# Kernel tuning notes

Hardware: AMD Instinct MI355X
Metric: run time of the kernel (lower is better)

Reference implementation:

```python
import jax, jax.numpy as jnp
import numpy as np

D = 2048          # input_dim == dec_hidden_size
S = 16384         # src_time_steps
H = 250           # projection hidden (hard-coded in module)


def setup_inputs() -> dict:
    key = jax.random.key(0)
    ks = jax.random.split(key, 12)
    sc_d = 1.0 / np.sqrt(D)
    sc_3d = 1.0 / np.sqrt(3 * D)
    sc_h = 1.0 / np.sqrt(H)
    return {
        "s_prev": jax.random.normal(ks[0], (1, 1, D), jnp.float32),
        "enc_hs": jax.random.normal(ks[1], (1, S, D), jnp.float32),
        "cur_men_rep": jax.random.normal(ks[2], (1, 1, D), jnp.float32),
        "src_mask": jax.random.randint(ks[3], (1, S), 0, 2, jnp.int32),
        "W_info": jax.random.normal(ks[4], (D, D), jnp.float32) * sc_d,
        "W_ctx": jax.random.normal(ks[5], (D, D), jnp.float32) * sc_d,
        "W_q": jax.random.normal(ks[6], (D, D), jnp.float32) * sc_d,
        "b_q": jnp.zeros((D,), jnp.float32),
        "W_p1": jax.random.normal(ks[7], (H, 3 * D), jnp.float32) * sc_3d,
        "b_p1": jnp.zeros((H,), jnp.float32),
        "W_p2": jax.random.normal(ks[8], (1, H), jnp.float32) * sc_h,
        "b_p2": jnp.zeros((1,), jnp.float32),
    }


def reference(s_prev, enc_hs, cur_men_rep, src_mask,
              W_info, W_ctx, W_q, b_q, W_p1, b_p1, W_p2, b_p2):
    # dh = linear_info(cur_men_rep): [1,1,D]; uh = linear_ctx(enc_hs): [1,S,D]
    dh = jnp.einsum('bqe,de->bqd', cur_men_rep, W_info)
    uh = jnp.einsum('bse,de->bsd', enc_hs, W_ctx)
    wq = jnp.einsum('bqe,de->bqd', s_prev, W_q) + b_q
    # cat(uh, wq.repeat, dh.repeat) -> tanh : [1,S,3D]
    wquh = jnp.tanh(jnp.concatenate(
        [uh, jnp.broadcast_to(wq, uh.shape), jnp.broadcast_to(dh, uh.shape)],
        axis=2))
    # projection: Linear(3D,250) -> Dropout(eval: identity) -> ReLU -> Linear(250,1)
    h = jax.nn.relu(jnp.einsum('bsk,hk->bsh', wquh, W_p1) + b_p1)
    scores = (jnp.einsum('bsh,oh->bso', h, W_p2) + b_p2).squeeze()   # [S] (B=1)
    scores = jnp.where(src_mask.squeeze().astype(bool), -jnp.inf, scores)
    attn = jax.nn.softmax(scores, axis=-1)                            # [S]
    ctx = jnp.sum(enc_hs * attn[None, :, None], axis=1)               # [1,D]
    return attn, ctx
```

## Files before the change

kernel.cpp:

```cpp
#include <hip/hip_runtime.h>
#include <hip/hip_bf16.h>
#include <stdint.h>

#define DD 2048
#define SS 16384
#define HH 250
#define GEMMB_GRID 264

typedef __attribute__((ext_vector_type(8))) short bf16x8;
typedef __attribute__((ext_vector_type(4))) short bf16x4;
typedef __attribute__((ext_vector_type(4))) float f32x4;

__device__ __forceinline__ unsigned short f2bf(float f){
  union { float f; uint32_t u; } v; v.f = f;
  uint32_t u = v.u;
  return (unsigned short)((u + 0x7fffu + ((u >> 16) & 1u)) >> 16);
}
__device__ __forceinline__ float bf2f(unsigned short h){
  union { uint32_t u; float f; } v; v.u = ((uint32_t)h) << 16; return v.f;
}
__device__ __forceinline__ bf16x4 pk4(float4 a){
  bf16x4 v;
  v[0]=(short)f2bf(a.x); v[1]=(short)f2bf(a.y); v[2]=(short)f2bf(a.z); v[3]=(short)f2bf(a.w);
  return v;
}
__device__ __forceinline__ float fast_tanh(float x){
  return 1.0f - 2.0f / (1.0f + __expf(2.0f * x));
}
__device__ __forceinline__ void gl_lds16(const void* g, void* l){
  __builtin_amdgcn_global_load_lds((const __attribute__((address_space(1))) void*)g,
                                   (__attribute__((address_space(3))) void*)l, 16, 0, 0);
}

__global__ __launch_bounds__(1024) void scan_kernel(const int* __restrict__ mask,
                                                    int* __restrict__ idx,
                                                    int* __restrict__ cpos,
                                                    int* __restrict__ mcount)
{
  __shared__ int wsum[16];
  const int t = threadIdx.x, lane = t & 63, w = t >> 6;
  int running = 0;
  for(int k = 0; k < 16; k++){
    const int e = k * 1024 + t;
    const int m = (mask[e] == 0);
    unsigned long long bal = __ballot(m);
    if(lane == 0) wsum[w] = __popcll(bal);
    __syncthreads();
    int wpre = 0;
    for(int i = 0; i < w; i++) wpre += wsum[i];
    int tot = wpre;
    for(int i = w; i < 16; i++) tot += wsum[i];
    const int lpre = __popcll(bal & ((1ull << lane) - 1ull));
    const int pos = running + wpre + lpre;
    if(m){ idx[pos] = e; cpos[e] = pos; } else cpos[e] = -1;
    running += tot;
    __syncthreads();
  }
  if(t == 0){
    mcount[0] = running;
    mcount[1] = (running + 255) & ~255;
    mcount[2] = (running + 63) & ~63;
  }
}

__global__ __launch_bounds__(256) void mega_kernel(
    const float* __restrict__ enc, unsigned short* __restrict__ encb,
    const float* __restrict__ W_ctx, unsigned short* __restrict__ wctxb,
    const float* __restrict__ W_p1, unsigned short* __restrict__ wp1ab,
    const float* __restrict__ s_prev, const float* __restrict__ cmr,
    const float* __restrict__ Wq, const float* __restrict__ bq,
    const float* __restrict__ Winfo,
    float* __restrict__ twq, float* __restrict__ tdh)
{
  const int b = blockIdx.x, t = threadIdx.x;
  if(b < 2048){
    const float4* in4 = (const float4*)enc;
    bf16x4* out4 = (bf16x4*)encb;
    const int gt = b * 256 + t;
    const int S = 524288;
    #pragma unroll
    for(int k = 0; k < 4; k++){
      int i0 = gt + (4 * k + 0) * S, i1 = gt + (4 * k + 1) * S;
      int i2 = gt + (4 * k + 2) * S, i3 = gt + (4 * k + 3) * S;
      float4 a = in4[i0], c = in4[i1], d = in4[i2], e = in4[i3];
      out4[i0] = pk4(a); out4[i1] = pk4(c); out4[i2] = pk4(d); out4[i3] = pk4(e);
    }
  } else if(b < 2304){
    const float4* in4 = (const float4*)W_ctx;
    bf16x4* out4 = (bf16x4*)wctxb;
    const int gt = (b - 2048) * 256 + t;
    const int S = 65536;
    #pragma unroll
    for(int k = 0; k < 4; k++){
      int i0 = gt + (4 * k + 0) * S, i1 = gt + (4 * k + 1) * S;
      int i2 = gt + (4 * k + 2) * S, i3 = gt + (4 * k + 3) * S;
      float4 a = in4[i0], c = in4[i1], d = in4[i2], e = in4[i3];
      out4[i0] = pk4(a); out4[i1] = pk4(c); out4[i2] = pk4(d); out4[i3] = pk4(e);
    }
  } else if(b < 2336){
    bf16x4* out4 = (bf16x4*)wp1ab;
    const int gt = (b - 2304) * 256 + t;
    const int S = 8192;
    #pragma unroll
    for(int k = 0; k < 16; k++){
      int i = gt + k * S;
      int row = i >> 9, col = i & 511;
      bf16x4 v;
      if(row < HH){
        float4 a = *(const float4*)(W_p1 + (size_t)row * (3 * DD) + (col << 2));
        v = pk4(a);
      } else {
        v[0] = 0; v[1] = 0; v[2] = 0; v[3] = 0;
      }
      out4[i] = v;
    }
  } else {
    int vb = b - 2336;
    int wid = t >> 6, lane = t & 63;
    bool isq = vb < 512;
    int r = (isq ? vb : vb - 512) * 4 + wid;
    const float* M = (isq ? Wq : Winfo) + (size_t)r * DD;
    const float* x = isq ? s_prev : cmr;
    float s = 0.f;
    for(int i = lane; i < DD; i += 64) s += M[i] * x[i];
    #pragma unroll
    for(int o = 32; o; o >>= 1) s += __shfl_xor(s, o);
    if(lane == 0){
      if(isq) twq[r] = fast_tanh(s + bq[r]);
      else    tdh[r] = fast_tanh(s);
    }
  }
}

__device__ __forceinline__ void stageA_idx(const unsigned short* __restrict__ g,
                                           const int* r2, int kt, char* ldsbase,
                                           int wid, int lane)
{
  const int srow = lane >> 3;
  const int c = (lane & 7) ^ srow;
  #pragma unroll
  for(int i = 0; i < 2; i++){
    int r8 = (wid * 2 + i) * 8;
    gl_lds16(g + (size_t)r2[i] * DD + kt + c * 8, ldsbase + r8 * 128);
  }
}
__device__ __forceinline__ void stage_half(const unsigned short* __restrict__ g,
                                           int grow0, int kt, char* ldsbase,
                                           int wid, int lane)
{
  const int srow = lane >> 3;
  const int c = (lane & 7) ^ srow;
  #pragma unroll
  for(int i = 0; i < 2; i++){
    int r8 = (wid * 2 + i) * 8;
    gl_lds16(g + (size_t)(grow0 + r8 + srow) * DD + kt + c * 8,
             ldsbase + r8 * 128);
  }
}
#define RDF(base, lr, kc) (*(const bf16x8*)((base) + (lr) * 128 + (((kc) * 16) ^ (((lr) & 7) << 4))))

__global__ __launch_bounds__(512, 2) void gemmA_kernel(
    const unsigned short* __restrict__ A, const int* __restrict__ idx,
    const unsigned short* __restrict__ B, const int* __restrict__ mcount,
    unsigned short* __restrict__ Ct,
    const float* __restrict__ wp1, const float* __restrict__ bp1,
    const float* __restrict__ twq, const float* __restrict__ tdh,
    float* __restrict__ bias2)
{
  const int tid = threadIdx.x, lane = tid & 63, wid = tid >> 6;
  if(blockIdx.x >= 512){
    int h = (blockIdx.x - 512) * 8 + wid;
    if(h >= HH){ if(lane == 0 && h < 256) bias2[h] = 0.f; return; }
    const float* r1 = wp1 + (size_t)h * (3 * DD) + DD;
    const float* r2 = wp1 + (size_t)h * (3 * DD) + 2 * DD;
    float s = 0.f;
    for(int i = lane; i < DD; i += 64) s += r1[i] * twq[i] + r2[i] * tdh[i];
    #pragma unroll
    for(int o = 32; o; o >>= 1) s += __shfl_xor(s, o);
    if(lane == 0) bias2[h] = s + bp1[h];
    return;
  }
  __shared__ alignas(128) char lds[131072];
  const int wm = wid >> 2, wn = wid & 3;
  const int slot = blockIdx.x >> 3;
  const int mt = (blockIdx.x & 7) + ((slot >> 3) << 3);
  const int n0 = (slot & 7) * 256;
  const int MT = mcount[1] >> 8;
  if(mt >= MT) return;
  const int m0 = mt * 256;
  const int frow = lane & 15, kch = lane >> 4;

  int ra0[2], ra1[2];
  {
    const int tot = mcount[0];
    const int srow = lane >> 3;
    #pragma unroll
    for(int i = 0; i < 2; i++){
      int r0 = m0 + (wid * 2 + i) * 8 + srow;
      int r1 = r0 + 128;
      ra0[i] = idx[r0 < tot ? r0 : tot - 1];
      ra1[i] = idx[r1 < tot ? r1 : tot - 1];
    }
  }

  f32x4 acc[8][4] = {};

  stageA_idx(A, ra0, 0, lds,         wid, lane);
  stageA_idx(A, ra1, 0, lds + 16384, wid, lane);
  stage_half(B, n0,        0, lds + 32768,         wid, lane);
  stage_half(B, n0 + 128,  0, lds + 49152,         wid, lane);
  stage_half(B, n0,       64, lds + 65536 + 32768, wid, lane);
  stage_half(B, n0 + 128, 64, lds + 65536 + 49152, wid, lane);
  asm volatile("s_waitcnt vmcnt(4)" ::: "memory");
  __builtin_amdgcn_s_barrier();

  #pragma unroll 2
  for(int t = 0; t < 32; t++){
    const int d = t & 1;
    char* Ab = lds + d * 65536;
    char* Bb = Ab + 32768;
    char* An = lds + (d ^ 1) * 65536;
    bf16x8 bfr[4][2];
    #pragma unroll
    for(int q = 0; q < 4; q++){
      if(q == 0){
        #pragma unroll
        for(int nr = 0; nr < 4; nr++){
          int row = wn * 64 + nr * 16 + frow;
          #pragma unroll
          for(int ks = 0; ks < 2; ks++) bfr[nr][ks] = RDF(Bb, row, ks * 4 + kch);
        }
      }
      bf16x8 afr[2][2];
      #pragma unroll
      for(int mi = 0; mi < 2; mi++){
        int row = wm * 128 + (q * 2 + mi) * 16 + frow;
        #pragma unroll
        for(int ks = 0; ks < 2; ks++) afr[mi][ks] = RDF(Ab, row, ks * 4 + kch);
      }
      if(q == 0){
        if(t + 1 < 32){
          stageA_idx(A, ra0, (t + 1) * 64, An,         wid, lane);
          stageA_idx(A, ra1, (t + 1) * 64, An + 16384, wid, lane);
        }
      } else if(q == 1){
        if(t + 2 < 32) stage_half(B, n0,       (t + 2) * 64, Bb,         wid, lane);
      } else if(q == 2){
        if(t + 2 < 32) stage_half(B, n0 + 128, (t + 2) * 64, Bb + 16384, wid, lane);
      }
      __builtin_amdgcn_s_barrier();
      __builtin_amdgcn_sched_barrier(0);
      __builtin_amdgcn_s_setprio(1);
      #pragma unroll
      for(int mi = 0; mi < 2; mi++)
        #pragma unroll
        for(int nr = 0; nr < 4; nr++)
          #pragma unroll
          for(int ks = 0; ks < 2; ks++)
            acc[q * 2 + mi][nr] = __builtin_amdgcn_mfma_f32_16x16x32_bf16(
                afr[mi][ks], bfr[nr][ks], acc[q * 2 + mi][nr], 0, 0, 0);
      __builtin_amdgcn_s_setprio(0);
      __builtin_amdgcn_sched_barrier(0);
      if(q == 3){
        if(t < 30)       asm volatile("s_waitcnt vmcnt(4)" ::: "memory");
        else if(t == 30) asm volatile("s_waitcnt vmcnt(0)" ::: "memory");
      }
      __builtin_amdgcn_s_barrier();
    }
  }

  const int r0 = m0 + wm * 128 + (lane >> 4) * 4;
  const int c0 = n0 + wn * 64 + frow;
  #pragma unroll
  for(int mr = 0; mr < 8; mr++)
    #pragma unroll
    for(int nr = 0; nr < 4; nr++)
      #pragma unroll
      for(int r = 0; r < 4; r++)
        Ct[(size_t)(r0 + mr * 16 + r) * DD + c0 + nr * 16] = f2bf(fast_tanh(acc[mr][nr][r]));
}

__global__ __launch_bounds__(512, 4) void gemmB_kernel(
    const unsigned short* __restrict__ A, const unsigned short* __restrict__ B,
    const int* __restrict__ mcount, const float* __restrict__ bias2,
    const float* __restrict__ w2, const float* __restrict__ bp2,
    float* __restrict__ attnc, float* __restrict__ Tpart)
{
  __shared__ alignas(128) char lds[81920];
  __shared__ float sred[8][32];
  const int tid = threadIdx.x, lane = tid & 63, wid = tid >> 6;
  const int wm = wid >> 2, wn = wid & 3;
  const int m0 = blockIdx.x * 64;
  const int mc0 = mcount[0], mc2 = mcount[2];
  if(m0 >= mc2){ if(tid == 0) Tpart[blockIdx.x] = 0.f; return; }
  const int frow = lane & 15, kch = lane >> 4;
  const int srow = lane >> 3, sc = ((lane & 7) ^ srow) * 8;

  f32x4 acc[2][4] = {};

  gl_lds16(A + (size_t)(m0 + wid * 8 + srow) * DD + sc, lds + wid * 1024);
  #pragma unroll
  for(int i = 0; i < 4; i++){
    int l = wid + 8 * i;
    gl_lds16(B + (size_t)(l * 8 + srow) * DD + sc,      lds + 16384 + l * 1024);
    gl_lds16(B + (size_t)(l * 8 + srow) * DD + 64 + sc, lds + 49152 + l * 1024);
  }
  asm volatile("s_waitcnt vmcnt(4)" ::: "memory");
  __builtin_amdgcn_s_barrier();

  #pragma unroll 2
  for(int t = 0; t < 32; t++){
    const int d = t & 1;
    char* Ab = lds + d * 8192;
    char* An = lds + (d ^ 1) * 8192;
    char* Bb = lds + 16384 + d * 32768;
    bf16x8 bfr[4][2], afr[2];
    #pragma unroll
    for(int q = 0; q < 2; q++){
      if(q == 0){
        #pragma unroll
        for(int nr = 0; nr < 4; nr++){
          int row = wn * 64 + nr * 16 + frow;
          #pragma unroll
          for(int ks = 0; ks < 2; ks++) bfr[nr][ks] = RDF(Bb, row, ks * 4 + kch);
        }
      }
      {
        int row = wm * 32 + q * 16 + frow;
        #pragma unroll
        for(int ks = 0; ks < 2; ks++) afr[ks] = RDF(Ab, row, ks * 4 + kch);
      }
      if(q == 0){
        if(t + 1 < 32)
          gl_lds16(A + (size_t)(m0 + wid * 8 + srow) * DD + (t + 1) * 64 + sc, An + wid * 1024);
      } else {
        if(t + 2 < 32){
          #pragma unroll
          for(int i = 0; i < 4; i++){
            int l = wid + 8 * i;
            gl_lds16(B + (size_t)(l * 8 + srow) * DD + (t + 2) * 64 + sc, Bb + l * 1024);
          }
        }
      }
      __builtin_amdgcn_s_barrier();
      __builtin_amdgcn_sched_barrier(0);
      __builtin_amdgcn_s_setprio(1);
      #pragma unroll
      for(int nr = 0; nr < 4; nr++)
        #pragma unroll
        for(int ks = 0; ks < 2; ks++)
          acc[q][nr] = __builtin_amdgcn_mfma_f32_16x16x32_bf16(afr[ks], bfr[nr][ks], acc[q][nr], 0, 0, 0);
      __builtin_amdgcn_s_setprio(0);
      __builtin_amdgcn_sched_barrier(0);
      if(q == 1){
        if(t < 30)       asm volatile("s_waitcnt vmcnt(4)" ::: "memory");
        else if(t == 30) asm volatile("s_waitcnt vmcnt(0)" ::: "memory");
      }
      __builtin_amdgcn_s_barrier();
    }
  }

  float w2v[4], b2v[4];
  #pragma unroll
  for(int in = 0; in < 4; in++){
    int n = wn * 64 + in * 16 + frow;
    w2v[in] = (n < HH) ? w2[n] : 0.f;
    b2v[in] = bias2[n];
  }
  #pragma unroll
  for(int mi = 0; mi < 2; mi++){
    #pragma unroll
    for(int r = 0; r < 4; r++){
      float s = 0.f;
      #pragma unroll
      for(int in = 0; in < 4; in++){
        float h = acc[mi][in][r] + b2v[in];
        s += (h > 0.f ? h : 0.f) * w2v[in];
      }
      s += __shfl_xor(s, 1); s += __shfl_xor(s, 2);
      s += __shfl_xor(s, 4); s += __shfl_xor(s, 8);
      if(frow == 0) sred[wid][mi * 16 + (lane >> 4) * 4 + r] = s;
    }
  }
  __syncthreads();
  if(tid < 64){
    int wmr = tid >> 5, rr = tid & 31;
    float s = sred[wmr * 4][rr] + sred[wmr * 4 + 1][rr] + sred[wmr * 4 + 2][rr]
            + sred[wmr * 4 + 3][rr] + bp2[0];
    int j = m0 + tid;
    float e = (j < mc0) ? __expf(s) : 0.f;
    if(j < mc0) attnc[j] = e;
    #pragma unroll
    for(int o = 32; o; o >>= 1) e += __shfl_xor(e, o);
    if(tid == 0) Tpart[blockIdx.x] = e;
  }
}

__global__ __launch_bounds__(256) void normctx_kernel(
    const float* __restrict__ attnc, const int* __restrict__ cpos,
    const int* __restrict__ idx, const int* __restrict__ mcount,
    const float* __restrict__ Tpart, const unsigned short* __restrict__ encb,
    float* __restrict__ out, float* __restrict__ part)
{
  const int b = blockIdx.x, t = threadIdx.x;
  if(b < 64){
    __shared__ float sT;
    if(t == 0){
      float s = 0.f;
      for(int i = 0; i < GEMMB_GRID; i++) s += Tpart[i];
      sT = 1.0f / s;
    }
    __syncthreads();
    int i = b * 256 + t;
    int cp = cpos[i];
    out[i] = (cp >= 0) ? attnc[cp] * sT : 0.f;
  } else {
    const int bb = b - 64;
    const int mc0 = mcount[0];
    const int chunk = (mc0 + 255) >> 8;
    const int j0 = bb * chunk;
    const int j1 = min(j0 + chunk, mc0);
    float a[8] = {};
    for(int j = j0; j < j1; j++){
      float e = attnc[j];
      bf16x8 v = *(const bf16x8*)(encb + (size_t)idx[j] * DD + t * 8);
      #pragma unroll
      for(int k = 0; k < 8; k++) a[k] += e * bf2f((unsigned short)v[k]);
    }
    float* o = part + (size_t)bb * DD + t * 8;
    #pragma unroll
    for(int k = 0; k < 8; k++) o[k] = a[k];
  }
}

__global__ __launch_bounds__(256) void ctxr_kernel(
    const float* __restrict__ part, const float* __restrict__ Tpart,
    float* __restrict__ out)
{
  __shared__ float sT;
  if(threadIdx.x == 0){
    float s = 0.f;
    for(int i = 0; i < GEMMB_GRID; i++) s += Tpart[i];
    sT = 1.0f / s;
  }
  __syncthreads();
  const int dcol = blockIdx.x * 256 + threadIdx.x;
  float s = 0.f;
  for(int b = 0; b < 256; b++) s += part[(size_t)b * DD + dcol];
  out[dcol] = s * sT;
}

extern "C" void kernel_launch(void* const* d_in, const int* in_sizes, int n_in,
                              void* d_out, int out_size, void* d_ws, size_t ws_size,
                              hipStream_t stream)
{
  const float* s_prev = (const float*)d_in[0];
  const float* enc    = (const float*)d_in[1];
  const float* cmr    = (const float*)d_in[2];
  const int*   mask   = (const int*)d_in[3];
  const float* W_info = (const float*)d_in[4];
  const float* W_ctx  = (const float*)d_in[5];
  const float* W_q    = (const float*)d_in[6];
  const float* b_q    = (const float*)d_in[7];
  const float* W_p1   = (const float*)d_in[8];
  const float* b_p1   = (const float*)d_in[9];
  const float* W_p2   = (const float*)d_in[10];
  const float* b_p2   = (const float*)d_in[11];
  float* out = (float*)d_out;

  char* ws = (char*)d_ws;
  unsigned short* encb    = (unsigned short*)(ws);
  unsigned short* tanhbuf = (unsigned short*)(ws + 67108864);
  unsigned short* wctxb   = (unsigned short*)(ws + 134217728);
  unsigned short* wp1ab   = (unsigned short*)(ws + 142606336);
  int*   idx    = (int*)(ws + 143654912);
  int*   cpos   = (int*)(ws + 143720448);
  float* attnc  = (float*)(ws + 143785984);
  float* part   = (float*)(ws + 143851520);
  float* twq    = (float*)(ws + 145948672);
  float* tdh    = (float*)(ws + 145956864);
  float* bias2  = (float*)(ws + 145965056);
  int*   mcount = (int*)(ws + 145966080);
  float* Tpart  = (float*)(ws + 145966208);

  mega_kernel<<<3360, 256, 0, stream>>>(enc, encb, W_ctx, wctxb, W_p1, wp1ab,
                                        s_prev, cmr, W_q, b_q, W_info, twq, tdh);
  scan_kernel<<<1, 1024, 0, stream>>>(mask, idx, cpos, mcount);
  gemmA_kernel<<<544, 512, 0, stream>>>(encb, idx, wctxb, mcount, tanhbuf,
                                        W_p1, b_p1, twq, tdh, bias2);
  gemmB_kernel<<<GEMMB_GRID, 512, 0, stream>>>(tanhbuf, wp1ab, mcount, bias2,
                                               W_p2, b_p2, attnc, Tpart);
  normctx_kernel<<<320, 256, 0, stream>>>(attnc, cpos, idx, mcount, Tpart,
                                          encb, out, part);
  ctxr_kernel<<<8, 256, 0, stream>>>(part, Tpart, out + SS);
}
```

Measured before the change: 216.8 us.

## Fuse enc fp32-to-bf16 conversion into gemmA loads, drop encb buffer

Removes the separate pass that converts the whole 128MB fp32 encoder tensor to bf16. gemmA now gathers fp32 rows through registers, converts them and writes them into swizzled LDS. normctx reads fp32 enc directly. This avoids a full read-plus-write pass over enc for masked-out rows too. The cost is that gemmA reads 2x bytes per A tile through VGPRs instead of direct-to-LDS loads, and takes on more register pressure and an extra LDS write step in its pipeline.

Result: slower. 249.4 us (+15.0%).

```diff
diff --git a/kernel.cpp b/kernel.cpp
--- a/kernel.cpp
+++ b/kernel.cpp
@@ -22,6 +22,16 @@
 __device__ __forceinline__ bf16x4 pk4(float4 a){
   bf16x4 v;
   v[0]=(short)f2bf(a.x); v[1]=(short)f2bf(a.y); v[2]=(short)f2bf(a.z); v[3]=(short)f2bf(a.w);
+  return v;
+}
+__device__ __forceinline__ bf16x8 pk8(float4 a, float4 c, bool alive){
+  bf16x8 v;
+  v[0]=(short)f2bf(a.x); v[1]=(short)f2bf(a.y); v[2]=(short)f2bf(a.z); v[3]=(short)f2bf(a.w);
+  v[4]=(short)f2bf(c.x); v[5]=(short)f2bf(c.y); v[6]=(short)f2bf(c.z); v[7]=(short)f2bf(c.w);
+  if(!alive){
+    #pragma unroll
+    for(int i = 0; i < 8; i++) v[i] = 0;
+  }
   return v;
 }
 __device__ __forceinline__ float fast_tanh(float x){
@@ -64,7 +74,6 @@
 }
 
 __global__ __launch_bounds__(256) void mega_kernel(
-    const float* __restrict__ enc, unsigned short* __restrict__ encb,
     const float* __restrict__ W_ctx, unsigned short* __restrict__ wctxb,
     const float* __restrict__ W_p1, unsigned short* __restrict__ wp1ab,
     const float* __restrict__ s_prev, const float* __restrict__ cmr,
@@ -73,49 +82,28 @@
     float* __restrict__ twq, float* __restrict__ tdh)
 {
   const int b = blockIdx.x, t = threadIdx.x;
-  if(b < 2048){
-    const float4* in4 = (const float4*)enc;
-    bf16x4* out4 = (bf16x4*)encb;
-    const int gt = b * 256 + t;
-    const int S = 524288;
-    #pragma unroll
-    for(int k = 0; k < 4; k++){
-      int i0 = gt + (4 * k + 0) * S, i1 = gt + (4 * k + 1) * S;
-      int i2 = gt + (4 * k + 2) * S, i3 = gt + (4 * k + 3) * S;
-      float4 a = in4[i0], c = in4[i1], d = in4[i2], e = in4[i3];
-      out4[i0] = pk4(a); out4[i1] = pk4(c); out4[i2] = pk4(d); out4[i3] = pk4(e);
-    }
-  } else if(b < 2304){
+  if(b < 256){
     const float4* in4 = (const float4*)W_ctx;
     bf16x4* out4 = (bf16x4*)wctxb;
-    const int gt = (b - 2048) * 256 + t;
-    const int S = 65536;
-    #pragma unroll
-    for(int k = 0; k < 4; k++){
-      int i0 = gt + (4 * k + 0) * S, i1 = gt + (4 * k + 1) * S;
-      int i2 = gt + (4 * k + 2) * S, i3 = gt + (4 * k + 3) * S;
-      float4 a = in4[i0], c = in4[i1], d = in4[i2], e = in4[i3];
-      out4[i0] = pk4(a); out4[i1] = pk4(c); out4[i2] = pk4(d); out4[i3] = pk4(e);
-    }
-  } else if(b < 2336){
+    const int gt = b * 256 + t;
+    for(int i = gt; i < 1048576; i += 65536) out4[i] = pk4(in4[i]);
+  } else if(b < 288){
     bf16x4* out4 = (bf16x4*)wp1ab;
-    const int gt = (b - 2304) * 256 + t;
-    const int S = 8192;
+    const int gt = (b - 256) * 256 + t;
     #pragma unroll
     for(int k = 0; k < 16; k++){
-      int i = gt + k * S;
+      int i = gt + k * 8192;
       int row = i >> 9, col = i & 511;
       bf16x4 v;
       if(row < HH){
-        float4 a = *(const float4*)(W_p1 + (size_t)row * (3 * DD) + (col << 2));
-        v = pk4(a);
+        v = pk4(*(const float4*)(W_p1 + (size_t)row * (3 * DD) + (col << 2)));
       } else {
         v[0] = 0; v[1] = 0; v[2] = 0; v[3] = 0;
       }
       out4[i] = v;
     }
   } else {
-    int vb = b - 2336;
+    int vb = b - 288;
     int wid = t >> 6, lane = t & 63;
     bool isq = vb < 512;
     int r = (isq ? vb : vb - 512) * 4 + wid;
@@ -132,18 +120,6 @@
   }
 }
 
-__device__ __forceinline__ void stageA_idx(const unsigned short* __restrict__ g,
-                                           const int* r2, int kt, char* ldsbase,
-                                           int wid, int lane)
-{
-  const int srow = lane >> 3;
-  const int c = (lane & 7) ^ srow;
-  #pragma unroll
-  for(int i = 0; i < 2; i++){
-    int r8 = (wid * 2 + i) * 8;
-    gl_lds16(g + (size_t)r2[i] * DD + kt + c * 8, ldsbase + r8 * 128);
-  }
-}
 __device__ __forceinline__ void stage_half(const unsigned short* __restrict__ g,
                                            int grow0, int kt, char* ldsbase,
                                            int wid, int lane)
@@ -160,7 +136,7 @@
 #define RDF(base, lr, kc) (*(const bf16x8*)((base) + (lr) * 128 + (((kc) * 16) ^ (((lr) & 7) << 4))))
 
 __global__ __launch_bounds__(512, 2) void gemmA_kernel(
-    const unsigned short* __restrict__ A, const int* __restrict__ idx,
+    const float* __restrict__ enc, const int* __restrict__ idx,
     const unsigned short* __restrict__ B, const int* __restrict__ mcount,
     unsigned short* __restrict__ Ct,
     const float* __restrict__ wp1, const float* __restrict__ bp1,
@@ -190,36 +166,39 @@
   const int m0 = mt * 256;
   const int frow = lane & 15, kch = lane >> 4;
 
-  int ra0[2], ra1[2];
-  {
-    const int tot = mcount[0];
-    const int srow = lane >> 3;
-    #pragma unroll
-    for(int i = 0; i < 2; i++){
-      int r0 = m0 + (wid * 2 + i) * 8 + srow;
-      int r1 = r0 + 128;
-      ra0[i] = idx[r0 < tot ? r0 : tot - 1];
-      ra1[i] = idx[r1 < tot ? r1 : tot - 1];
-    }
-  }
+  const int p = lane & 1;
+  const int r_loc = wid * 32 + (lane >> 1);
+  const int mc0 = mcount[0];
+  const bool alive = (m0 + r_loc) < mc0;
+  const int ridx = alive ? idx[m0 + r_loc] : idx[0];
+  const float* rp = enc + (size_t)ridx * DD + p * 32;
+  int wroff[4];
+  #pragma unroll
+  for(int j = 0; j < 4; j++)
+    wroff[j] = r_loc * 128 + (((p * 4 + j) * 16) ^ ((r_loc & 7) << 4));
 
   f32x4 acc[8][4] = {};
-
-  stageA_idx(A, ra0, 0, lds,         wid, lane);
-  stageA_idx(A, ra1, 0, lds + 16384, wid, lane);
-  stage_half(B, n0,        0, lds + 32768,         wid, lane);
-  stage_half(B, n0 + 128,  0, lds + 49152,         wid, lane);
-  stage_half(B, n0,       64, lds + 65536 + 32768, wid, lane);
-  stage_half(B, n0 + 128, 64, lds + 65536 + 49152, wid, lane);
+  float4 ld[8];
+
+  #pragma unroll
+  for(int j = 0; j < 8; j++) ld[j] = *(const float4*)(rp + j * 4);
+  stage_half(B, n0,        0, lds + 65536,         wid, lane);
+  stage_half(B, n0 + 128,  0, lds + 65536 + 16384, wid, lane);
+  stage_half(B, n0,       64, lds + 98304,         wid, lane);
+  stage_half(B, n0 + 128, 64, lds + 98304 + 16384, wid, lane);
+  #pragma unroll
+  for(int j = 0; j < 4; j++)
+    *(bf16x8*)(lds + wroff[j]) = pk8(ld[2 * j], ld[2 * j + 1], alive);
+  asm volatile("s_waitcnt lgkmcnt(0)" ::: "memory");
   asm volatile("s_waitcnt vmcnt(4)" ::: "memory");
   __builtin_amdgcn_s_barrier();
 
   #pragma unroll 2
   for(int t = 0; t < 32; t++){
     const int d = t & 1;
-    char* Ab = lds + d * 65536;
-    char* Bb = Ab + 32768;
-    char* An = lds + (d ^ 1) * 65536;
+    char* Ab = lds + d * 32768;
+    char* An = lds + (d ^ 1) * 32768;
+    char* Bb = lds + 65536 + d * 32768;
     bf16x8 bfr[4][2];
     #pragma unroll
     for(int q = 0; q < 4; q++){
@@ -240,8 +219,8 @@
       }
       if(q == 0){
         if(t + 1 < 32){
-          stageA_idx(A, ra0, (t + 1) * 64, An,         wid, lane);
-          stageA_idx(A, ra1, (t + 1) * 64, An + 16384, wid, lane);
+          #pragma unroll
+          for(int j = 0; j < 8; j++) ld[j] = *(const float4*)(rp + (t + 1) * 64 + j * 4);
         }
       } else if(q == 1){
         if(t + 2 < 32) stage_half(B, n0,       (t + 2) * 64, Bb,         wid, lane);
@@ -262,8 +241,13 @@
       __builtin_amdgcn_s_setprio(0);
       __builtin_amdgcn_sched_barrier(0);
       if(q == 3){
-        if(t < 30)       asm volatile("s_waitcnt vmcnt(4)" ::: "memory");
-        else if(t == 30) asm volatile("s_waitcnt vmcnt(0)" ::: "memory");
+        if(t + 1 < 32){
+          #pragma unroll
+          for(int j = 0; j < 4; j++)
+            *(bf16x8*)(An + wroff[j]) = pk8(ld[2 * j], ld[2 * j + 1], alive);
+        }
+        asm volatile("s_waitcnt lgkmcnt(0)" ::: "memory");
+        asm volatile("s_waitcnt vmcnt(4)" ::: "memory");
       }
       __builtin_amdgcn_s_barrier();
     }
@@ -399,7 +383,7 @@
 __global__ __launch_bounds__(256) void normctx_kernel(
     const float* __restrict__ attnc, const int* __restrict__ cpos,
     const int* __restrict__ idx, const int* __restrict__ mcount,
-    const float* __restrict__ Tpart, const unsigned short* __restrict__ encb,
+    const float* __restrict__ Tpart, const float* __restrict__ enc,
     float* __restrict__ out, float* __restrict__ part)
 {
   const int b = blockIdx.x, t = threadIdx.x;
@@ -423,9 +407,10 @@
     float a[8] = {};
     for(int j = j0; j < j1; j++){
       float e = attnc[j];
-      bf16x8 v = *(const bf16x8*)(encb + (size_t)idx[j] * DD + t * 8);
-      #pragma unroll
-      for(int k = 0; k < 8; k++) a[k] += e * bf2f((unsigned short)v[k]);
+      const float4* p4 = (const float4*)(enc + (size_t)idx[j] * DD + t * 8);
+      float4 x = p4[0], y = p4[1];
+      a[0] += e * x.x; a[1] += e * x.y; a[2] += e * x.z; a[3] += e * x.w;
+      a[4] += e * y.x; a[5] += e * y.y; a[6] += e * y.z; a[7] += e * y.w;
     }
     float* o = part + (size_t)bb * DD + t * 8;
     #pragma unroll
@@ -469,28 +454,27 @@
   float* out = (float*)d_out;
 
   char* ws = (char*)d_ws;
-  unsigned short* encb    = (unsigned short*)(ws);
-  unsigned short* tanhbuf = (unsigned short*)(ws + 67108864);
-  unsigned short* wctxb   = (unsigned short*)(ws + 134217728);
-  unsigned short* wp1ab   = (unsigned short*)(ws + 142606336);
-  int*   idx    = (int*)(ws + 143654912);
-  int*   cpos   = (int*)(ws + 143720448);
-  float* attnc  = (float*)(ws + 143785984);
-  float* part   = (float*)(ws + 143851520);
-  float* twq    = (float*)(ws + 145948672);
-  float* tdh    = (float*)(ws + 145956864);
-  float* bias2  = (float*)(ws + 145965056);
-  int*   mcount = (int*)(ws + 145966080);
-  float* Tpart  = (float*)(ws + 145966208);
-
-  mega_kernel<<<3360, 256, 0, stream>>>(enc, encb, W_ctx, wctxb, W_p1, wp1ab,
+  unsigned short* tanhbuf = (unsigned short*)(ws);
+  unsigned short* wctxb   = (unsigned short*)(ws + 67108864);
+  unsigned short* wp1ab   = (unsigned short*)(ws + 75497472);
+  int*   idx    = (int*)(ws + 76546048);
+  int*   cpos   = (int*)(ws + 76611584);
+  float* attnc  = (float*)(ws + 76677120);
+  float* part   = (float*)(ws + 76742656);
+  float* twq    = (float*)(ws + 78839808);
+  float* tdh    = (float*)(ws + 78848000);
+  float* bias2  = (float*)(ws + 78856192);
+  int*   mcount = (int*)(ws + 78857216);
+  float* Tpart  = (float*)(ws + 78857344);
+
+  mega_kernel<<<1312, 256, 0, stream>>>(W_ctx, wctxb, W_p1, wp1ab,
                                         s_prev, cmr, W_q, b_q, W_info, twq, tdh);
   scan_kernel<<<1, 1024, 0, stream>>>(mask, idx, cpos, mcount);
-  gemmA_kernel<<<544, 512, 0, stream>>>(encb, idx, wctxb, mcount, tanhbuf,
+  gemmA_kernel<<<544, 512, 0, stream>>>(enc, idx, wctxb, mcount, tanhbuf,
                                         W_p1, b_p1, twq, tdh, bias2);
   gemmB_kernel<<<GEMMB_GRID, 512, 0, stream>>>(tanhbuf, wp1ab, mcount, bias2,
                                                W_p2, b_p2, attnc, Tpart);
   normctx_kernel<<<320, 256, 0, stream>>>(attnc, cpos, idx, mcount, Tpart,
-                                          encb, out, part);
+                                          enc, out, part);
   ctxr_kernel<<<8, 256, 0, stream>>>(part, Tpart, out + SS);
 }
```
